# Kernel optimization log

Hardware: AMD Instinct MI355X
Metric: run time of the kernel (lower is better)

Reference implementation:

```python
import jax, jax.numpy as jnp
import numpy as np

FRAME_LEN = 512
FRAME_HOP = 256
EPSILON = float(np.finfo(np.float32).eps)


def _dft_kernels(frame_len=FRAME_LEN):
    # Matches torch: K = view_as_real(fft.rfft(eye(N), dim=1))[:frame_len], windowed by hann.
    # rfft of delta at t gives exp(-2pi i f t / N): real = cos, imag = -sin.
    N = frame_len  # already a power of two
    n = jnp.arange(frame_len, dtype=jnp.float32)
    window = 0.5 * (1.0 - jnp.cos(2.0 * jnp.pi * n / frame_len))  # periodic hann
    f = jnp.arange(N // 2 + 1, dtype=jnp.float32)  # 257 bins
    ang = 2.0 * jnp.pi * f[:, None] * n[None, :] / N  # [F, L]
    Kr = jnp.cos(ang) * window
    Ki = -jnp.sin(ang) * window  # torch rfft imaginary part
    return Kr, Ki


def _frame(x, frame_len=FRAME_LEN, hop=FRAME_HOP):
    B, Ns = x.shape
    T = (Ns - frame_len) // hop + 1
    idx = jnp.arange(T)[:, None] * hop + jnp.arange(frame_len)[None, :]  # [T, L]
    return x[:, idx]  # [B, T, L]


def reference(x):
    Kr, Ki = _dft_kernels()
    xf = _frame(x)  # [B, T, L]
    r = jnp.einsum('btl,fl->bft', xf, Kr)       # real part of conv1d output
    i = -jnp.einsum('btl,fl->bft', xf, Ki)      # i = -imag (as in torch code)
    mag = jnp.sqrt(r * r + i * i)               # B x F x T
    f = jnp.clip(mag, EPSILON, None)
    mean = jnp.mean(f, axis=-1, keepdims=True)
    std = jnp.std(f, axis=-1, keepdims=True, ddof=1)  # torch std is unbiased
    feat = (f - mean) / (std + EPSILON)
    return mag, feat


def setup_inputs() -> dict:
    key = jax.random.key(0)
    x = jax.random.normal(key, (64, 160000), dtype=jnp.float32)
    return {"x": x}
```

## Files before the change

### kernel.cpp

```cpp
#include <hip/hip_runtime.h>
#include <math.h>

#define FRAME_LEN 512
#define HOP       256
#define NFREQ     257
#define NBATCH    64
#define NSAMP     160000
#define NSAMPH    80000
#define TFRAMES   624
#define EPS       1.1920928955078125e-07f

#define MT 128
#define FT 32
#define BK 64
#define KH 256
#define XBLKS 5000

#define ASZ (MT * BK)
#define BSZ (2 * FT * BK)

typedef __attribute__((ext_vector_type(8))) short short8;
typedef __attribute__((ext_vector_type(4))) float f32x4;

static __device__ __forceinline__ unsigned int f2bf(float f) {
    unsigned int u = __float_as_uint(f);
    return (u + 0x7fffu + ((u >> 16) & 1u)) >> 16;
}
static __device__ __forceinline__ void gload_lds16(const void* g, void* l) {
    __builtin_amdgcn_global_load_lds(
        (const __attribute__((address_space(1))) void*)g,
        (__attribute__((address_space(3))) void*)l, 16, 0, 0);
}

__global__ __launch_bounds__(256) void prep(const float* __restrict__ x,
                                            unsigned short* __restrict__ xe,
                                            unsigned short* __restrict__ xo,
                                            unsigned short* __restrict__ Wec,
                                            unsigned short* __restrict__ Wes,
                                            unsigned short* __restrict__ Woc,
                                            unsigned short* __restrict__ Wos) {
    if (blockIdx.x < XBLKS) {
        int i = blockIdx.x * 256 + threadIdx.x;
        const float4* src = (const float4*)x + (size_t)i * 2;
        float4 a = src[0], b = src[1];
        uint2 e, o;
        e.x = f2bf(a.x) | (f2bf(a.z) << 16);
        e.y = f2bf(b.x) | (f2bf(b.z) << 16);
        o.x = f2bf(a.y) | (f2bf(a.w) << 16);
        o.y = f2bf(b.y) | (f2bf(b.w) << 16);
        *(uint2*)(xe + (size_t)i * 4) = e;
        *(uint2*)(xo + (size_t)i * 4) = o;
    } else {
        int f = blockIdx.x - XBLKS;
        int n2 = threadIdx.x;
        unsigned short ec = 0, es = 0, oc = 0, os = 0;
        if (f <= 128) {
            int ne = 2 * n2, no = 2 * n2 + 1;
            float we = 0.5f * (1.0f - cosf(2.0f * (float)M_PI * (float)ne / (float)FRAME_LEN));
            float wo = 0.5f * (1.0f - cosf(2.0f * (float)M_PI * (float)no / (float)FRAME_LEN));
            float ange = (float)((f * ne) & (FRAME_LEN - 1)) * (2.0f * (float)M_PI / (float)FRAME_LEN);
            float ango = (float)((f * no) & (FRAME_LEN - 1)) * (2.0f * (float)M_PI / (float)FRAME_LEN);
            float se_, ce_, so_, co_;
            sincosf(ange, &se_, &ce_);
            sincosf(ango, &so_, &co_);
            ec = (unsigned short)f2bf(ce_ * we);
            es = (unsigned short)f2bf(se_ * we);
            oc = (unsigned short)f2bf(co_ * wo);
            os = (unsigned short)f2bf(so_ * wo);
        }
        Wec[f * KH + n2] = ec; Wes[f * KH + n2] = es;
        Woc[f * KH + n2] = oc; Wos[f * KH + n2] = os;
    }
}

__global__ __launch_bounds__(256) void stft_mfma(
    const unsigned short* __restrict__ xe, const unsigned short* __restrict__ xo,
    const unsigned short* __restrict__ Wec, const unsigned short* __restrict__ Wes,
    const unsigned short* __restrict__ Woc, const unsigned short* __restrict__ Wos,
    float* __restrict__ mag)
{
    __shared__ unsigned short As[2][MT][BK];
    __shared__ unsigned short Bs[2][2][FT][BK];

    const int tid = threadIdx.x;
    const int logical = ((int)blockIdx.x & 7) * 195 + ((int)blockIdx.x >> 3);
    const int tileM = logical / 5;
    const int tileF = logical % 5;
    const int wid = tid >> 6;
    const int lane = tid & 63;
    const int lrow = lane & 15;
    const int lhi = lane >> 4;

    unsigned short* AsB = &As[0][0][0];
    unsigned short* BsB = &Bs[0][0][0][0];

    const unsigned short* pA[2][4];
    #pragma unroll
    for (int j = 0; j < 4; j++) {
        int idx = wid * 4 + j;
        int row = idx * 8 + (lane >> 3);
        int m = tileM * MT + row;
        int b = m / TFRAMES;
        int t = m - b * TFRAMES;
        int chunk = (lane & 7) ^ (row & 7);
        size_t off = (size_t)b * NSAMPH + t * (HOP / 2) + chunk * 8;
        pA[0][j] = xe + off;
        pA[1][j] = xo + off;
    }
    const unsigned short* pB[2][2];
    #pragma unroll
    for (int j = 0; j < 2; j++) {
        int i = wid * 2 + j;
        int row = (i & 3) * 8 + (lane >> 3);
        int fg = tileF * FT + row;
        int chunk = (lane & 7) ^ (row & 7);
        size_t off = (size_t)fg * KH + chunk * 8;
        pB[0][j] = ((i & 4) ? Wes : Wec) + off;
        pB[1][j] = ((i & 4) ? Wos : Woc) + off;
    }

    f32x4 aC[2][2][2] = {};
    f32x4 aS[2][2][2] = {};

    #pragma unroll
    for (int j = 0; j < 4; j++)
        gload_lds16(pA[0][j], AsB + (wid * 4 + j) * 512);
    #pragma unroll
    for (int j = 0; j < 2; j++)
        gload_lds16(pB[0][j], BsB + (wid * 2 + j) * 512);
    __syncthreads();

    int buf = 0;
    #pragma unroll
    for (int it = 0; it < 8; it++) {
        const int p = it >> 2;
        if (it < 7) {
            const int pn = (it + 1) >> 2;
            const int k0 = ((it + 1) & 3) * BK;
            #pragma unroll
            for (int j = 0; j < 4; j++)
                gload_lds16(pA[pn][j] + k0, AsB + (buf ^ 1) * ASZ + (wid * 4 + j) * 512);
            #pragma unroll
            for (int j = 0; j < 2; j++)
                gload_lds16(pB[pn][j] + k0, BsB + (buf ^ 1) * BSZ + (wid * 2 + j) * 512);
        }
        #pragma unroll
        for (int ks = 0; ks < 2; ks++) {
            short8 a[2], bc[2], bsn[2];
            const int c = (ks * 4 + lhi) ^ (lrow & 7);
            #pragma unroll
            for (int mf = 0; mf < 2; mf++)
                a[mf] = *(const short8*)(AsB + buf * ASZ +
                    (wid * 32 + mf * 16 + lrow) * BK + c * 8);
            #pragma unroll
            for (int nf = 0; nf < 2; nf++) {
                bc[nf]  = *(const short8*)(BsB + buf * BSZ +
                    (nf * 16 + lrow) * BK + c * 8);
                bsn[nf] = *(const short8*)(BsB + buf * BSZ + FT * BK +
                    (nf * 16 + lrow) * BK + c * 8);
            }
            #pragma unroll
            for (int mf = 0; mf < 2; mf++) {
                #pragma unroll
                for (int nf = 0; nf < 2; nf++) {
                    aC[p][mf][nf] = __builtin_amdgcn_mfma_f32_16x16x32_bf16(
                        a[mf], bc[nf], aC[p][mf][nf], 0, 0, 0);
                    aS[p][mf][nf] = __builtin_amdgcn_mfma_f32_16x16x32_bf16(
                        a[mf], bsn[nf], aS[p][mf][nf], 0, 0, 0);
                }
            }
        }
        __syncthreads();
        buf ^= 1;
    }

    #pragma unroll
    for (int mf = 0; mf < 2; mf++) {
        int m0 = tileM * MT + wid * 32 + mf * 16 + lhi * 4;
        int b = m0 / TFRAMES;
        int t = m0 - b * TFRAMES;
        #pragma unroll
        for (int nf = 0; nf < 2; nf++) {
            int f = tileF * FT + nf * 16 + lrow;
            float4 od, om;
            #pragma unroll
            for (int q = 0; q < 4; q++) {
                const float Ce = aC[0][mf][nf][q], Co = aC[1][mf][nf][q];
                const float Se = aS[0][mf][nf][q], So = aS[1][mf][nf][q];
                const float rd = Ce + Co, id = Se + So;
                const float rm = Ce - Co, im = So - Se;
                (&od.x)[q] = sqrtf(rd * rd + id * id);
                (&om.x)[q] = sqrtf(rm * rm + im * im);
            }
            if (f <= 128)
                *(float4*)(mag + ((size_t)b * NFREQ + f) * TFRAMES + t) = od;
            if (f <= 127)
                *(float4*)(mag + ((size_t)b * NFREQ + (256 - f)) * TFRAMES + t) = om;
        }
    }
}

__global__ __launch_bounds__(256) void normalize(const float* __restrict__ mag,
                                                 float* __restrict__ feat)
{
    const int row = blockIdx.x * 4 + (threadIdx.x >> 6);
    const int lane = threadIdx.x & 63;
    const float* mp = mag + (size_t)row * TFRAMES;

    float4 v[3];
    float sum = 0.f;
    #pragma unroll
    for (int i = 0; i < 3; i++) {
        int c4 = lane + i * 64;
        if (c4 < TFRAMES / 4) {
            float4 t = *(const float4*)(mp + c4 * 4);
            t.x = fmaxf(t.x, EPS); t.y = fmaxf(t.y, EPS);
            t.z = fmaxf(t.z, EPS); t.w = fmaxf(t.w, EPS);
            v[i] = t;
            sum += (t.x + t.y) + (t.z + t.w);
        } else {
            v[i] = make_float4(0.f, 0.f, 0.f, 0.f);
        }
    }
    #pragma unroll
    for (int off = 1; off < 64; off <<= 1) sum += __shfl_xor(sum, off, 64);
    const float mean = sum * (1.0f / (float)TFRAMES);

    float ssd = 0.f;
    #pragma unroll
    for (int i = 0; i < 3; i++) {
        int c4 = lane + i * 64;
        if (c4 < TFRAMES / 4) {
            float dx = v[i].x - mean, dy = v[i].y - mean;
            float dz = v[i].z - mean, dw = v[i].w - mean;
            ssd += (dx * dx + dy * dy) + (dz * dz + dw * dw);
        }
    }
    #pragma unroll
    for (int off = 1; off < 64; off <<= 1) ssd += __shfl_xor(ssd, off, 64);
    const float stdv = sqrtf(ssd * (1.0f / (float)(TFRAMES - 1)));
    const float inv = 1.0f / (stdv + EPS);

    float* fp = feat + (size_t)row * TFRAMES;
    #pragma unroll
    for (int i = 0; i < 3; i++) {
        int c4 = lane + i * 64;
        if (c4 < TFRAMES / 4) {
            float4 o;
            o.x = (v[i].x - mean) * inv; o.y = (v[i].y - mean) * inv;
            o.z = (v[i].z - mean) * inv; o.w = (v[i].w - mean) * inv;
            *(float4*)(fp + c4 * 4) = o;
        }
    }
}

extern "C" void kernel_launch(void* const* d_in, const int* in_sizes, int n_in,
                              void* d_out, int out_size, void* d_ws, size_t ws_size,
                              hipStream_t stream) {
    const float* x = (const float*)d_in[0];
    unsigned short* Wec = (unsigned short*)d_ws;
    unsigned short* Wes = Wec + 160 * KH;
    unsigned short* Woc = Wes + 160 * KH;
    unsigned short* Wos = Woc + 160 * KH;
    unsigned short* xe  = Wos + 160 * KH;
    unsigned short* xo  = xe + (size_t)NBATCH * NSAMPH;
    float* mag  = (float*)d_out;
    float* feat = mag + (size_t)NBATCH * NFREQ * TFRAMES;

    prep<<<XBLKS + 160, 256, 0, stream>>>(x, xe, xo, Wec, Wes, Woc, Wos);

    stft_mfma<<<312 * 5, 256, 0, stream>>>(xe, xo, Wec, Wes, Woc, Wos, mag);

    normalize<<<NBATCH * NFREQ / 4, 256, 0, stream>>>(mag, feat);
}
```

Measured before the change: 54.40 us.

## Pre-tile framed signal in MFMA fragment order and load A directly to registers

The prep kernel now writes the bf16 signal into a pre-framed, fragment-ordered layout (each sample duplicated into two overlapping frames), so the STFT GEMM kernel can load A operands straight from global memory into registers with 16-byte loads. This drops the A-tile LDS staging and its share of LDS traffic and shared memory, and adds a launch-bounds occupancy hint of 3 blocks. The cost is doubling the bf16 signal workspace writes in prep and exposing global-load latency for A inside the k-loop without double buffering.

```diff
diff --git a/kernel.cpp b/kernel.cpp
--- a/kernel.cpp
+++ b/kernel.cpp
@@ -6,18 +6,15 @@
 #define NFREQ     257
 #define NBATCH    64
 #define NSAMP     160000
-#define NSAMPH    80000
 #define TFRAMES   624
 #define EPS       1.1920928955078125e-07f
 
 #define MT 128
 #define FT 32
-#define BK 64
 #define KH 256
 #define XBLKS 5000
-
-#define ASZ (MT * BK)
-#define BSZ (2 * FT * BK)
+#define BSZ (2 * FT * 64)
+
 
 typedef __attribute__((ext_vector_type(8))) short short8;
 typedef __attribute__((ext_vector_type(4))) float f32x4;
@@ -33,23 +30,40 @@
 }
 
 __global__ __launch_bounds__(256) void prep(const float* __restrict__ x,
-                                            unsigned short* __restrict__ xe,
-                                            unsigned short* __restrict__ xo,
+                                            unsigned short* __restrict__ xT,
                                             unsigned short* __restrict__ Wec,
                                             unsigned short* __restrict__ Wes,
                                             unsigned short* __restrict__ Woc,
                                             unsigned short* __restrict__ Wos) {
     if (blockIdx.x < XBLKS) {
-        int i = blockIdx.x * 256 + threadIdx.x;
-        const float4* src = (const float4*)x + (size_t)i * 2;
-        float4 a = src[0], b = src[1];
+        const int i = blockIdx.x * 256 + threadIdx.x;
+        const int g = i * 8;
+        const int b = g / NSAMP;
+        const int s = g - b * NSAMP;
+        const float4* src = (const float4*)(x + (size_t)b * NSAMP + s);
+        const float4 v0 = src[0], v1 = src[1];
         uint2 e, o;
-        e.x = f2bf(a.x) | (f2bf(a.z) << 16);
-        e.y = f2bf(b.x) | (f2bf(b.z) << 16);
-        o.x = f2bf(a.y) | (f2bf(a.w) << 16);
-        o.y = f2bf(b.y) | (f2bf(b.w) << 16);
-        *(uint2*)(xe + (size_t)i * 4) = e;
-        *(uint2*)(xo + (size_t)i * 4) = o;
+        e.x = f2bf(v0.x) | (f2bf(v0.z) << 16);
+        e.y = f2bf(v1.x) | (f2bf(v1.z) << 16);
+        o.x = f2bf(v0.y) | (f2bf(v0.w) << 16);
+        o.y = f2bf(v1.y) | (f2bf(v1.w) << 16);
+        const int t0 = s >> 8;
+        const int k0 = s & 255;
+        const int ch = k0 >> 6;
+        const int cpos = (k0 >> 1) & 31;
+        if (t0 < TFRAMES) {
+            size_t base = ((((size_t)(b * 39 + (t0 >> 4)) * 2) * 8 + ch) * 512)
+                          + (t0 & 15) * 32 + cpos;
+            *(uint2*)(xT + base) = e;
+            *(uint2*)(xT + base + 4096) = o;
+        }
+        const int t1 = t0 - 1;
+        if (t1 >= 0) {
+            size_t base = ((((size_t)(b * 39 + (t1 >> 4)) * 2) * 8 + (ch + 4)) * 512)
+                          + (t1 & 15) * 32 + cpos;
+            *(uint2*)(xT + base) = e;
+            *(uint2*)(xT + base + 4096) = o;
+        }
     } else {
         int f = blockIdx.x - XBLKS;
         int n2 = threadIdx.x;
@@ -73,14 +87,13 @@
     }
 }
 
-__global__ __launch_bounds__(256) void stft_mfma(
-    const unsigned short* __restrict__ xe, const unsigned short* __restrict__ xo,
+__global__ __launch_bounds__(256, 3) void stft_mfma(
+    const unsigned short* __restrict__ xT,
     const unsigned short* __restrict__ Wec, const unsigned short* __restrict__ Wes,
     const unsigned short* __restrict__ Woc, const unsigned short* __restrict__ Wos,
     float* __restrict__ mag)
 {
-    __shared__ unsigned short As[2][MT][BK];
-    __shared__ unsigned short Bs[2][2][FT][BK];
+    __shared__ unsigned short Bs[2][2][FT][64];
 
     const int tid = threadIdx.x;
     const int logical = ((int)blockIdx.x & 7) * 195 + ((int)blockIdx.x >> 3);
@@ -91,21 +104,13 @@
     const int lrow = lane & 15;
     const int lhi = lane >> 4;
 
-    unsigned short* AsB = &As[0][0][0];
     unsigned short* BsB = &Bs[0][0][0][0];
 
-    const unsigned short* pA[2][4];
-    #pragma unroll
-    for (int j = 0; j < 4; j++) {
-        int idx = wid * 4 + j;
-        int row = idx * 8 + (lane >> 3);
-        int m = tileM * MT + row;
-        int b = m / TFRAMES;
-        int t = m - b * TFRAMES;
-        int chunk = (lane & 7) ^ (row & 7);
-        size_t off = (size_t)b * NSAMPH + t * (HOP / 2) + chunk * 8;
-        pA[0][j] = xe + off;
-        pA[1][j] = xo + off;
+    const unsigned short* pA[2];
+    #pragma unroll
+    for (int mf = 0; mf < 2; mf++) {
+        int msub = tileM * 8 + wid * 2 + mf;
+        pA[mf] = xT + (size_t)msub * 8192 + lrow * 32 + lhi * 8;
     }
     const unsigned short* pB[2][2];
     #pragma unroll
@@ -123,9 +128,6 @@
     f32x4 aS[2][2][2] = {};
 
     #pragma unroll
-    for (int j = 0; j < 4; j++)
-        gload_lds16(pA[0][j], AsB + (wid * 4 + j) * 512);
-    #pragma unroll
     for (int j = 0; j < 2; j++)
         gload_lds16(pB[0][j], BsB + (wid * 2 + j) * 512);
     __syncthreads();
@@ -134,39 +136,40 @@
     #pragma unroll
     for (int it = 0; it < 8; it++) {
         const int p = it >> 2;
+        const int kc = it & 3;
         if (it < 7) {
             const int pn = (it + 1) >> 2;
-            const int k0 = ((it + 1) & 3) * BK;
-            #pragma unroll
-            for (int j = 0; j < 4; j++)
-                gload_lds16(pA[pn][j] + k0, AsB + (buf ^ 1) * ASZ + (wid * 4 + j) * 512);
+            const int kn = ((it + 1) & 3) * 64;
             #pragma unroll
             for (int j = 0; j < 2; j++)
-                gload_lds16(pB[pn][j] + k0, BsB + (buf ^ 1) * BSZ + (wid * 2 + j) * 512);
+                gload_lds16(pB[pn][j] + kn, BsB + (buf ^ 1) * BSZ + (wid * 2 + j) * 512);
+        }
+        short8 a0[2], a1[2];
+        #pragma unroll
+        for (int mf = 0; mf < 2; mf++) {
+            a0[mf] = *(const short8*)(pA[mf] + (size_t)(p * 8 + kc * 2 + 0) * 512);
+            a1[mf] = *(const short8*)(pA[mf] + (size_t)(p * 8 + kc * 2 + 1) * 512);
         }
         #pragma unroll
         for (int ks = 0; ks < 2; ks++) {
-            short8 a[2], bc[2], bsn[2];
-            const int c = (ks * 4 + lhi) ^ (lrow & 7);
-            #pragma unroll
-            for (int mf = 0; mf < 2; mf++)
-                a[mf] = *(const short8*)(AsB + buf * ASZ +
-                    (wid * 32 + mf * 16 + lrow) * BK + c * 8);
+            short8 bc[2], bsn[2];
+            const int ci = (ks * 4 + lhi) ^ (lrow & 7);
             #pragma unroll
             for (int nf = 0; nf < 2; nf++) {
                 bc[nf]  = *(const short8*)(BsB + buf * BSZ +
-                    (nf * 16 + lrow) * BK + c * 8);
-                bsn[nf] = *(const short8*)(BsB + buf * BSZ + FT * BK +
-                    (nf * 16 + lrow) * BK + c * 8);
+                    (nf * 16 + lrow) * 64 + ci * 8);
+                bsn[nf] = *(const short8*)(BsB + buf * BSZ + FT * 64 +
+                    (nf * 16 + lrow) * 64 + ci * 8);
             }
             #pragma unroll
             for (int mf = 0; mf < 2; mf++) {
+                const short8 a = ks ? a1[mf] : a0[mf];
                 #pragma unroll
                 for (int nf = 0; nf < 2; nf++) {
                     aC[p][mf][nf] = __builtin_amdgcn_mfma_f32_16x16x32_bf16(
-                        a[mf], bc[nf], aC[p][mf][nf], 0, 0, 0);
+                        a, bc[nf], aC[p][mf][nf], 0, 0, 0);
                     aS[p][mf][nf] = __builtin_amdgcn_mfma_f32_16x16x32_bf16(
-                        a[mf], bsn[nf], aS[p][mf][nf], 0, 0, 0);
+                        a, bsn[nf], aS[p][mf][nf], 0, 0, 0);
                 }
             }
         }
@@ -262,14 +265,13 @@
     unsigned short* Wes = Wec + 160 * KH;
     unsigned short* Woc = Wes + 160 * KH;
     unsigned short* Wos = Woc + 160 * KH;
-    unsigned short* xe  = Wos + 160 * KH;
-    unsigned short* xo  = xe + (size_t)NBATCH * NSAMPH;
+    unsigned short* xT  = Wos + 160 * KH;
     float* mag  = (float*)d_out;
     float* feat = mag + (size_t)NBATCH * NFREQ * TFRAMES;
 
-    prep<<<XBLKS + 160, 256, 0, stream>>>(x, xe, xo, Wec, Wes, Woc, Wos);
-
-    stft_mfma<<<312 * 5, 256, 0, stream>>>(xe, xo, Wec, Wes, Woc, Wos, mag);
+    prep<<<XBLKS + 160, 256, 0, stream>>>(x, xT, Wec, Wes, Woc, Wos);
+
+    stft_mfma<<<312 * 5, 256, 0, stream>>>(xT, Wec, Wes, Woc, Wos, mag);
 
     normalize<<<NBATCH * NFREQ / 4, 256, 0, stream>>>(mag, feat);
 }
```

Result: slower. 58.62 us (+7.8%).
